# Performance work log

Hardware: AMD Instinct MI355X
Metric: run time of the kernel (lower is better)

Reference implementation:

```python
import jax, jax.numpy as jnp
import numpy as np

SEQ, B, V, E, H, L, S_SRC = 128, 32, 32000, 1024, 1024, 3, 64


def setup_inputs() -> dict:
    key = jax.random.key(0)
    ks = jax.random.split(key, 8)
    sc = 0.05
    return {
        "tokens": jax.random.randint(ks[0], (SEQ, B), 0, V),
        "emb_W": jax.random.normal(ks[1], (V, E), jnp.float32) * 0.1,
        "W_ih": jax.random.normal(ks[2], (L, 4 * H, E), jnp.float32) * sc,
        "W_hh": jax.random.normal(ks[3], (L, 4 * H, H), jnp.float32) * sc,
        "b_ih": jnp.zeros((L, 4 * H), jnp.float32),
        "b_hh": jnp.zeros((L, 4 * H), jnp.float32),
        "attn_Win": jax.random.normal(ks[4], (E, E), jnp.float32) * sc,
        "attn_Wout": jax.random.normal(ks[5], (E, 2 * E), jnp.float32) * sc,
        "final_b": jnp.zeros((V,), jnp.float32),
        "encoder_outs": jax.random.normal(ks[6], (S_SRC, B, E), jnp.float32),
        "h0": jnp.zeros((L, B, H), jnp.float32),
        "c0": jnp.zeros((L, B, H), jnp.float32),
    }


def reference(tokens, emb_W, W_ih, W_hh, b_ih, b_hh, attn_Win, attn_Wout,
              final_b, encoder_outs, h0, c0):
    # Eval mode: all dropouts (dropoute/i/h/out) are identity.
    emb = emb_W[tokens]                                  # [SEQ, B, E]
    ctx = jnp.transpose(encoder_outs, (1, 0, 2))         # [B, S_src, E]

    def lstm_cell(x, h, c, l):
        gates = x @ W_ih[l].T + b_ih[l] + h @ W_hh[l].T + b_hh[l]  # [B, 4H]
        i, f, g, o = jnp.split(gates, 4, axis=-1)        # torch order: i,f,g,o
        i, f, o = jax.nn.sigmoid(i), jax.nn.sigmoid(f), jax.nn.sigmoid(o)
        g = jnp.tanh(g)
        c_new = f * c + i * g
        return o * jnp.tanh(c_new), c_new

    def step(carry, x_t):
        h, c = carry                                     # each [L, B, H]
        hs, cs = [], []
        inp = x_t
        for l in range(L):
            h_new, c_new = lstm_cell(inp, h[l], c[l], l)
            hs.append(h_new)
            cs.append(c_new)
            inp = h_new                                  # dropouth is identity
        # SoftDotAttention on last layer hidden
        target = h_new @ attn_Win.T                      # [B, E]
        attn = jax.nn.softmax(jnp.einsum('bse,be->bs', ctx, target), axis=-1)
        wc = jnp.einsum('bs,bse->be', attn, ctx)         # weighted context
        h_tilde = jnp.tanh(jnp.concatenate([wc, h_new], axis=-1) @ attn_Wout.T)
        return (jnp.stack(hs), jnp.stack(cs)), h_tilde

    (_, _), outs = jax.lax.scan(step, (h0, c0), emb)     # outs: [SEQ, B, E]
    logits = outs @ emb_W.T + final_b                    # tied weights: [SEQ, B, V]
    return logits
```

## Files before the change

### kernel.cpp

```cpp
#include <hip/hip_runtime.h>
#include <cstdint>
#include <cstddef>

#define SEQ   128
#define BB    32
#define EE    1024
#define HH    1024
#define G4    4096
#define VV    32000
#define NROWS 4096

typedef _Float16 h16x8 __attribute__((ext_vector_type(8)));
typedef _Float16 h16x4 __attribute__((ext_vector_type(4)));
typedef float f32x4  __attribute__((ext_vector_type(4)));

#define AS_G(p) ((const __attribute__((address_space(1))) void*)(p))
#define AS_L(p) ((__attribute__((address_space(3))) void*)(p))

__device__ __forceinline__ float sigmf(float x) { return 1.0f / (1.0f + expf(-x)); }

#define OFF_SYNC    0ull
#define OFF_HFRAG   40960ull
#define OFF_EMB     434176ull
#define OFF_X0      8822784ull
#define OFF_WIH0    42377216ull
#define OFF_WP4     50765824ull
#define OFF_WP0     84320256ull
#define OFF_EMBW    92708864ull
#define OFF_WIN     158244864ull
#define OFF_WOUT    160342016ull
#define OFF_ENC     164536320ull
#define OFF_H2ALL   168730624ull
#define OFF_CONCAT  177119232ull
#define OFF_TARGET  193896448ull
#define OFF_HT      202285056ull
#define WS_NEEDED   210673664ull

__global__ __launch_bounds__(256) void k_conv(const float* __restrict__ s,
                                              _Float16* __restrict__ d, int n4) {
  int i = blockIdx.x * blockDim.x + threadIdx.x;
  int st = gridDim.x * blockDim.x;
  for (; i < n4; i += st) {
    float4 v = ((const float4*)s)[i];
    h16x4 o; o[0] = (_Float16)v.x; o[1] = (_Float16)v.y; o[2] = (_Float16)v.z; o[3] = (_Float16)v.w;
    ((h16x4*)d)[i] = o;
  }
}

__global__ __launch_bounds__(256) void k_gather(const int* __restrict__ tok,
                                                const float* __restrict__ embW,
                                                _Float16* __restrict__ emb) {
  int row = blockIdx.x;
  int t = tok[row];
  float4 v = ((const float4*)(embW + (size_t)t * EE))[threadIdx.x];
  h16x4 o; o[0] = (_Float16)v.x; o[1] = (_Float16)v.y; o[2] = (_Float16)v.z; o[3] = (_Float16)v.w;
  ((h16x4*)(emb + (size_t)row * EE))[threadIdx.x] = o;
}

__global__ __launch_bounds__(256) void k_packw4(const float* __restrict__ Wih,
                                                const float* __restrict__ Whh,
                                                _Float16* __restrict__ out) {
  int i = blockIdx.x * blockDim.x + threadIdx.x;
  int st = gridDim.x * blockDim.x;
  const int total = 256 * 65536;
  for (; i < total; i += st) {
    int w = i >> 16, rem = i & 65535;
    int mat = rem >> 14, jj = (rem >> 10) & 15, k = rem & 1023;
    int layer = 1 + (mat >> 1), isHH = mat & 1;
    int row = ((jj >> 2) << 10) + (w << 2) + (jj & 3);
    int ks = k ^ ((jj & 7) << 3);
    const float* src = (isHH ? Whh : Wih) + (size_t)layer * G4 * 1024 + (size_t)row * 1024 + ks;
    out[i] = (_Float16)(*src);
  }
}

__global__ __launch_bounds__(256) void k_packw0(const float* __restrict__ Whh,
                                                _Float16* __restrict__ out) {
  int i = blockIdx.x * blockDim.x + threadIdx.x;
  int st = gridDim.x * blockDim.x;
  const int total = 256 * 16384;
  for (; i < total; i += st) {
    int w = i >> 14, rem = i & 16383;
    int ks = rem >> 9, lane = (rem >> 3) & 63, e = rem & 7;
    int jj = lane & 15, q = lane >> 4;
    int row = ((jj >> 2) << 10) + (w << 2) + (jj & 3);
    int k = ks * 32 + q * 8 + e;
    out[i] = (_Float16)Whh[(size_t)row * 1024 + k];
  }
}

__global__ __launch_bounds__(256) void k_init(const float* __restrict__ h0,
                                              _Float16* __restrict__ hfrag,
                                              unsigned* __restrict__ sync) {
  int i = blockIdx.x * blockDim.x + threadIdx.x;
  if (i < 64 + 8192) sync[i] = 0u;
  if (i >= 3 * BB * HH) return;
  int l = i >> 15, rem = i & 32767;
  int b = rem >> 10, n = rem & 1023;
  int parI = (l == 1) ? 0 : 1;
  int tbb = b >> 4, ks = n >> 5, q = (n >> 3) & 3, e = n & 7;
  int lane2 = (b & 15) | (q << 4);
  hfrag[(size_t)(l * 2 + parI) * 32768 + ((size_t)(tbb * 32 + ks) * 64 + lane2) * 8 + e] =
      (_Float16)h0[i];
}

template <int EPI>
__global__ __launch_bounds__(256) void k_gemm(const _Float16* __restrict__ A,
                                              const _Float16* __restrict__ B,
                                              void* __restrict__ C, int M, int N, int K,
                                              const float* __restrict__ bias1,
                                              const float* __restrict__ bias2) {
  __shared__ _Float16 As[2][128 * 32];
  __shared__ _Float16 Bs[2][128 * 32];
  const int ntn = N / 128;
  const int nwg = gridDim.x;
  const int bid = (blockIdx.x & 7) * (nwg >> 3) + (blockIdx.x >> 3);
  const int tm = bid / ntn, tn = bid % ntn;
  const int tid = threadIdx.x, lane = tid & 63;
  const int wv = tid >> 6, wr = wv >> 1, wc = wv & 1;
  f32x4 acc[4][4] = {};

  auto stage = [&](int buf, int k0) {
#pragma unroll
    for (int i = 0; i < 2; ++i) {
      int eo = (i * 256 + tid) * 8;
      int r = eo >> 5, c = eo & 31;
      __builtin_amdgcn_global_load_lds(AS_G(A + (size_t)(tm * 128 + r) * K + k0 + c),
                                       AS_L(&As[buf][eo]), 16, 0, 0);
      __builtin_amdgcn_global_load_lds(AS_G(B + (size_t)(tn * 128 + r) * K + k0 + c),
                                       AS_L(&Bs[buf][eo]), 16, 0, 0);
    }
  };
  stage(0, 0);
  __syncthreads();
  const int nk = K / 32;
  for (int kt = 0; kt < nk; ++kt) {
    if (kt + 1 < nk) stage((kt + 1) & 1, (kt + 1) * 32);
    const int buf = kt & 1;
    h16x8 af[4], bfr[4];
#pragma unroll
    for (int mi = 0; mi < 4; ++mi)
      af[mi] = *(const h16x8*)&As[buf][(wr * 64 + mi * 16 + (lane & 15)) * 32 + (lane >> 4) * 8];
#pragma unroll
    for (int ni = 0; ni < 4; ++ni)
      bfr[ni] = *(const h16x8*)&Bs[buf][(wc * 64 + ni * 16 + (lane & 15)) * 32 + (lane >> 4) * 8];
#pragma unroll
    for (int mi = 0; mi < 4; ++mi)
#pragma unroll
      for (int ni = 0; ni < 4; ++ni)
        acc[mi][ni] = __builtin_amdgcn_mfma_f32_16x16x32_f16(af[mi], bfr[ni], acc[mi][ni], 0, 0, 0);
    __syncthreads();
  }
  const int rbase = tm * 128 + wr * 64;
  const int cbase = tn * 128 + wc * 64;
#pragma unroll
  for (int mi = 0; mi < 4; ++mi) {
#pragma unroll
    for (int ni = 0; ni < 4; ++ni) {
#pragma unroll
      for (int r = 0; r < 4; ++r) {
        int mm = rbase + mi * 16 + (lane >> 4) * 4 + r;
        int nn = cbase + ni * 16 + (lane & 15);
        float v = acc[mi][ni][r];
        if (EPI == 1) {
          ((_Float16*)C)[(size_t)mm * N + nn] = (_Float16)v;
        } else {
          ((_Float16*)C)[(size_t)mm * N + nn] = (_Float16)tanhf(v);
        }
      }
    }
  }
}

template <int EPI>
__global__ __launch_bounds__(512, 2) void k_gemm256(const _Float16* __restrict__ A,
                                                    const _Float16* __restrict__ B,
                                                    void* __restrict__ C, int M, int N, int K,
                                                    const float* __restrict__ bias1,
                                                    const float* __restrict__ bias2) {
  extern __shared__ char glds[];
  _Float16* Asl = (_Float16*)glds;
  _Float16* Bsl = (_Float16*)(glds + 3 * 8192 * 2);
  const int ntn = N / 256;
  const int nwg = gridDim.x;
  const int bid = (blockIdx.x & 7) * (nwg >> 3) + (blockIdx.x >> 3);
  const int tm = bid / ntn, tn = bid % ntn;
  const int tid = threadIdx.x, lane = tid & 63;
  const int wid = tid >> 6, wm = wid >> 2, wn = wid & 3;
  const int fr = lane & 15, fc = lane >> 4;
  const int srow0 = tid >> 2, sg = tid & 3;

  f32x4 acc[8][4] = {};
  const int nt = K / 32;

  auto stage = [&](int t) {
    const int slot = t % 3;
    const size_t kof = (size_t)t * 32 + sg * 8;
#pragma unroll
    for (int r = 0; r < 2; ++r) {
      int row = r * 128 + srow0;
      __builtin_amdgcn_global_load_lds(AS_G(A + (size_t)(tm * 256 + row) * K + kof),
                                       AS_L(&Asl[slot * 8192 + row * 32 + sg * 8]), 16, 0, 0);
    }
#pragma unroll
    for (int r = 0; r < 2; ++r) {
      int row = r * 128 + srow0;
      __builtin_amdgcn_global_load_lds(AS_G(B + (size_t)(tn * 256 + row) * K + kof),
                                       AS_L(&Bsl[slot * 8192 + row * 32 + sg * 8]), 16, 0, 0);
    }
  };

  stage(0);
  stage(1);
  asm volatile("s_waitcnt vmcnt(4)" ::: "memory");
  asm volatile("s_barrier" ::: "memory");

  for (int t = 0; t < nt; ++t) {
    if (t + 2 < nt) {
      stage(t + 2);
      asm volatile("s_waitcnt vmcnt(4)" ::: "memory");
    } else {
      asm volatile("s_waitcnt vmcnt(0)" ::: "memory");
    }
    asm volatile("s_barrier" ::: "memory");
    const int slot = t % 3;
    const _Float16* as = &Asl[slot * 8192];
    const _Float16* bs = &Bsl[slot * 8192];
    h16x8 af[8], bf[4];
#pragma unroll
    for (int mi = 0; mi < 8; ++mi)
      af[mi] = *(const h16x8*)&as[(wm * 128 + mi * 16 + fr) * 32 + fc * 8];
#pragma unroll
    for (int ni = 0; ni < 4; ++ni)
      bf[ni] = *(const h16x8*)&bs[(wn * 64 + ni * 16 + fr) * 32 + fc * 8];
    __builtin_amdgcn_s_setprio(1);
#pragma unroll
    for (int mi = 0; mi < 8; ++mi)
#pragma unroll
      for (int ni = 0; ni < 4; ++ni)
        acc[mi][ni] = __builtin_amdgcn_mfma_f32_16x16x32_f16(af[mi], bf[ni], acc[mi][ni], 0, 0, 0);
    __builtin_amdgcn_s_setprio(0);
    asm volatile("s_barrier" ::: "memory");
  }

  const int rbase = tm * 256 + wm * 128;
  const int cbase = tn * 256 + wn * 64;
#pragma unroll
  for (int mi = 0; mi < 8; ++mi) {
#pragma unroll
    for (int ni = 0; ni < 4; ++ni) {
#pragma unroll
      for (int r = 0; r < 4; ++r) {
        int mm = rbase + mi * 16 + fc * 4 + r;
        int nn = cbase + ni * 16 + fr;
        float v = acc[mi][ni][r];
        if (EPI == 0) {
          ((float*)C)[(size_t)mm * N + nn] = v + bias1[nn];
        } else {
          ((_Float16*)C)[(size_t)mm * N + nn] = (_Float16)(v + bias1[nn] + bias2[nn]);
        }
      }
    }
  }
}

__global__ __launch_bounds__(512) void k_recur(const _Float16* __restrict__ Wp4,
                                               const _Float16* __restrict__ Wp0,
                                               const _Float16* __restrict__ X0bf,
                                               _Float16* __restrict__ hfrag,
                                               _Float16* __restrict__ h2all,
                                               _Float16* __restrict__ concat,
                                               const float* __restrict__ bih,
                                               const float* __restrict__ bhh,
                                               const float* __restrict__ c0p,
                                               unsigned* __restrict__ sync) {
  extern __shared__ char lds[];
  _Float16* ldsW = (_Float16*)lds;
  float* redbuf = (float*)(lds + 131072);
  _Float16* hstage = (_Float16*)(lds + 131072);
  float* gbuf = (float*)(lds + 149504);
  unsigned* arrive = sync + 64;

  const int w = blockIdx.x;
  const int tid = threadIdx.x, lane = tid & 63, wv = tid >> 6;
  const int tb = wv & 1, kq = wv >> 1;
  const int row = (lane >> 4) * 4, col = lane & 15;

  for (int i = 0; i < 16; ++i) {
    int eo = (i * 512 + tid) * 8;
    *(h16x8*)&ldsW[eo] = *(const h16x8*)(Wp4 + (size_t)w * 65536 + eo);
  }
  h16x8 w0reg[8];
#pragma unroll
  for (int i = 0; i < 8; ++i)
    w0reg[i] = *(const h16x8*)(Wp0 + (size_t)w * 16384 + ((size_t)(kq * 8 + i) * 64 + lane) * 8);

  const int eb = tid >> 2, eni = tid & 3, en = w * 4 + eni;
  float c0r = 0.f, c1r = 0.f, c2r = 0.f;
  float b1r[4] = {0, 0, 0, 0}, b2r[4] = {0, 0, 0, 0};
  if (tid < 128) {
    c0r = c0p[0 * BB * HH + eb * HH + en];
    c1r = c0p[1 * BB * HH + eb * HH + en];
    c2r = c0p[2 * BB * HH + eb * HH + en];
#pragma unroll
    for (int g = 0; g < 4; ++g) {
      b1r[g] = bih[1 * G4 + g * 1024 + en] + bhh[1 * G4 + g * 1024 + en];
      b2r[g] = bih[2 * G4 + g * 1024 + en] + bhh[2 * G4 + g * 1024 + en];
    }
  }
  const int pk_l = tid >> 5, pk_r = tid & 31;
  const size_t pk_idx = ((size_t)(((pk_r >> 4) * 32 + (w >> 3)) * 64 + (pk_r & 15) +
                                  (((w >> 1) & 3) << 4))) * 8 + 4 * (w & 1);
  __syncthreads();

  for (int tau = 0; tau < 130; ++tau) {
    const int p = tau & 1;
    const _Float16* h0r = hfrag + (size_t)(0 + (1 - p)) * 32768;
    const _Float16* h1r = hfrag + (size_t)(2 + (1 - p)) * 32768;
    const _Float16* h2r = hfrag + (size_t)(4 + (1 - p)) * 32768;

    h16x8 a0[8], a1[8], a2[8];
#pragma unroll
    for (int i = 0; i < 8; ++i) {
      int ks = kq * 8 + i;
      size_t off = ((size_t)(tb * 32 + ks) * 64 + lane) * 8;
      a0[i] = *(const h16x8*)(h0r + off);
      a1[i] = *(const h16x8*)(h1r + off);
      a2[i] = *(const h16x8*)(h2r + off);
    }
    float xg0 = 0.f, xg1 = 0.f, xg2 = 0.f, xg3 = 0.f;
    if (tid < 128 && tau < 128) {
      size_t xb = ((size_t)(tau * BB + eb)) * G4 + en;
      xg0 = (float)X0bf[xb];        xg1 = (float)X0bf[xb + 1024];
      xg2 = (float)X0bf[xb + 2048]; xg3 = (float)X0bf[xb + 3072];
    }
    f32x4 acc0 = {}, acc1 = {}, acc2 = {};
#pragma unroll
    for (int i = 0; i < 8; ++i) {
      int ks = kq * 8 + i;
      int jj = lane & 15, q = lane >> 4;
      int kk = (ks * 32 + q * 8) ^ ((jj & 7) << 3);
      const h16x8 bw1i = *(const h16x8*)&ldsW[0 * 16384 + jj * 1024 + kk];
      const h16x8 bw1h = *(const h16x8*)&ldsW[1 * 16384 + jj * 1024 + kk];
      const h16x8 bw2i = *(const h16x8*)&ldsW[2 * 16384 + jj * 1024 + kk];
      const h16x8 bw2h = *(const h16x8*)&ldsW[3 * 16384 + jj * 1024 + kk];
      acc0 = __builtin_amdgcn_mfma_f32_16x16x32_f16(a0[i], w0reg[i], acc0, 0, 0, 0);
      acc1 = __builtin_amdgcn_mfma_f32_16x16x32_f16(a0[i], bw1i, acc1, 0, 0, 0);
      acc1 = __builtin_amdgcn_mfma_f32_16x16x32_f16(a1[i], bw1h, acc1, 0, 0, 0);
      acc2 = __builtin_amdgcn_mfma_f32_16x16x32_f16(a1[i], bw2i, acc2, 0, 0, 0);
      acc2 = __builtin_amdgcn_mfma_f32_16x16x32_f16(a2[i], bw2h, acc2, 0, 0, 0);
    }
    if (kq >= 1) {
      int s = kq - 1;
#pragma unroll
      for (int r = 0; r < 4; ++r) {
        redbuf[((0 * 3 + s) * 2 + tb) * 256 + (row + r) * 16 + col] = acc0[r];
        redbuf[((1 * 3 + s) * 2 + tb) * 256 + (row + r) * 16 + col] = acc1[r];
        redbuf[((2 * 3 + s) * 2 + tb) * 256 + (row + r) * 16 + col] = acc2[r];
      }
    }
    __syncthreads();
    if (kq == 0) {
#pragma unroll
      for (int r = 0; r < 4; ++r) {
        float v0 = acc0[r], v1 = acc1[r], v2 = acc2[r];
#pragma unroll
        for (int s = 0; s < 3; ++s) {
          v0 += redbuf[((0 * 3 + s) * 2 + tb) * 256 + (row + r) * 16 + col];
          v1 += redbuf[((1 * 3 + s) * 2 + tb) * 256 + (row + r) * 16 + col];
          v2 += redbuf[((2 * 3 + s) * 2 + tb) * 256 + (row + r) * 16 + col];
        }
        gbuf[(0 * 32 + tb * 16 + row + r) * 16 + col] = v0;
        gbuf[(1 * 32 + tb * 16 + row + r) * 16 + col] = v1;
        gbuf[(2 * 32 + tb * 16 + row + r) * 16 + col] = v2;
      }
    }
    __syncthreads();
    if (tid < 128) {
      if (tau < 128) {
        float gi = gbuf[(0 * 32 + eb) * 16 + eni] + xg0;
        float gf = gbuf[(0 * 32 + eb) * 16 + 4 + eni] + xg1;
        float gg = gbuf[(0 * 32 + eb) * 16 + 8 + eni] + xg2;
        float go = gbuf[(0 * 32 + eb) * 16 + 12 + eni] + xg3;
        c0r = sigmf(gf) * c0r + sigmf(gi) * tanhf(gg);
        hstage[0 * 128 + tid] = (_Float16)(sigmf(go) * tanhf(c0r));
      }
      if (tau >= 1 && tau < 129) {
        float gi = gbuf[(1 * 32 + eb) * 16 + eni] + b1r[0];
        float gf = gbuf[(1 * 32 + eb) * 16 + 4 + eni] + b1r[1];
        float gg = gbuf[(1 * 32 + eb) * 16 + 8 + eni] + b1r[2];
        float go = gbuf[(1 * 32 + eb) * 16 + 12 + eni] + b1r[3];
        c1r = sigmf(gf) * c1r + sigmf(gi) * tanhf(gg);
        hstage[1 * 128 + tid] = (_Float16)(sigmf(go) * tanhf(c1r));
      }
      if (tau >= 2) {
        float gi = gbuf[(2 * 32 + eb) * 16 + eni] + b2r[0];
        float gf = gbuf[(2 * 32 + eb) * 16 + 4 + eni] + b2r[1];
        float gg = gbuf[(2 * 32 + eb) * 16 + 8 + eni] + b2r[2];
        float go = gbuf[(2 * 32 + eb) * 16 + 12 + eni] + b2r[3];
        c2r = sigmf(gf) * c2r + sigmf(gi) * tanhf(gg);
        float h = sigmf(go) * tanhf(c2r);
        _Float16 hb = (_Float16)h;
        hstage[2 * 128 + tid] = hb;
        int t2 = tau - 2;
        h2all[(size_t)(t2 * BB + eb) * HH + en] = hb;
        concat[(size_t)(t2 * BB + eb) * 2048 + 1024 + en] = hb;
      }
    }
    __syncthreads();
    {
      bool act = (tid < 96) &&
                 ((pk_l == 0) ? (tau < 128)
                  : (pk_l == 1) ? (tau >= 1 && tau < 129) : (tau >= 2));
      if (act) {
        unsigned long long v = *(const unsigned long long*)&hstage[pk_l * 128 + pk_r * 4];
        __hip_atomic_store(
            (unsigned long long*)(hfrag + (size_t)(pk_l * 2 + p) * 32768 + pk_idx), v,
            __ATOMIC_RELAXED, __HIP_MEMORY_SCOPE_AGENT);
      }
      asm volatile("s_waitcnt vmcnt(0)" ::: "memory");
    }
    __syncthreads();
    if (tid == 0)
      __hip_atomic_store(&arrive[w * 32], (unsigned)(tau + 1), __ATOMIC_RELAXED,
                         __HIP_MEMORY_SCOPE_AGENT);
    if (tau < 129) {
      if (tid < 64) {
        for (;;) {
          bool ok = true;
#pragma unroll
          for (int j = 0; j < 4; ++j) {
            unsigned v = __hip_atomic_load(&arrive[(tid * 4 + j) * 32], __ATOMIC_RELAXED,
                                           __HIP_MEMORY_SCOPE_AGENT);
            ok &= (v >= (unsigned)(tau + 1));
          }
          if (__all(ok)) break;
          __builtin_amdgcn_s_sleep(1);
        }
        __builtin_amdgcn_fence(__ATOMIC_ACQUIRE, "agent");
      }
      __syncthreads();
    }
  }
}

__global__ __launch_bounds__(256) void k_attn(const _Float16* __restrict__ target,
                                              const _Float16* __restrict__ encb,
                                              _Float16* __restrict__ concat) {
  __shared__ float sc[64];
  __shared__ float att[64];
  int m = blockIdx.x, b = m & 31;
  int tid = threadIdx.x, lane = tid & 63, wv = tid >> 6;
  const h16x8* tp = (const h16x8*)(target + (size_t)m * EE + lane * 16);
  h16x8 tg0 = tp[0], tg1 = tp[1];
  for (int si = 0; si < 16; ++si) {
    int s = wv * 16 + si;
    const h16x8* ep = (const h16x8*)(encb + ((size_t)s * BB + b) * EE + lane * 16);
    h16x8 e0 = ep[0], e1 = ep[1];
    float a = 0.f;
#pragma unroll
    for (int j = 0; j < 8; ++j) a += (float)e0[j] * (float)tg0[j];
#pragma unroll
    for (int j = 0; j < 8; ++j) a += (float)e1[j] * (float)tg1[j];
#pragma unroll
    for (int off = 32; off >= 1; off >>= 1) a += __shfl_xor(a, off);
    if (lane == 0) sc[s] = a;
  }
  __syncthreads();
  if (wv == 0) {
    float v = sc[lane], mx = v;
#pragma unroll
    for (int off = 32; off >= 1; off >>= 1) mx = fmaxf(mx, __shfl_xor(mx, off));
    float e = expf(v - mx), sm = e;
#pragma unroll
    for (int off = 32; off >= 1; off >>= 1) sm += __shfl_xor(sm, off);
    att[lane] = e / sm;
  }
  __syncthreads();
  int e4 = tid * 4;
  float a0 = 0, a1 = 0, a2 = 0, a3 = 0;
  for (int s = 0; s < 64; ++s) {
    float wgt = att[s];
    h16x4 ev = *(const h16x4*)(encb + ((size_t)s * BB + b) * EE + e4);
    a0 += wgt * (float)ev[0]; a1 += wgt * (float)ev[1];
    a2 += wgt * (float)ev[2]; a3 += wgt * (float)ev[3];
  }
  h16x4 o; o[0] = (_Float16)a0; o[1] = (_Float16)a1; o[2] = (_Float16)a2; o[3] = (_Float16)a3;
  *(h16x4*)(concat + (size_t)m * 2048 + e4) = o;
}

extern "C" void kernel_launch(void* const* d_in, const int* in_sizes, int n_in,
                              void* d_out, int out_size, void* d_ws, size_t ws_size,
                              hipStream_t stream) {
  const int* tokens = (const int*)d_in[0];
  const float* embW = (const float*)d_in[1];
  const float* Wih = (const float*)d_in[2];
  const float* Whh = (const float*)d_in[3];
  const float* bih = (const float*)d_in[4];
  const float* bhh = (const float*)d_in[5];
  const float* Win = (const float*)d_in[6];
  const float* Wout = (const float*)d_in[7];
  const float* finalb = (const float*)d_in[8];
  const float* enc = (const float*)d_in[9];
  const float* h0 = (const float*)d_in[10];
  const float* c0 = (const float*)d_in[11];
  (void)in_sizes; (void)n_in; (void)out_size;
  if (ws_size < WS_NEEDED) return;

  char* ws = (char*)d_ws;
  unsigned* sync = (unsigned*)(ws + OFF_SYNC);
  _Float16* hfrag = (_Float16*)(ws + OFF_HFRAG);
  _Float16* emb = (_Float16*)(ws + OFF_EMB);
  _Float16* X0bf = (_Float16*)(ws + OFF_X0);
  _Float16* Wih0b = (_Float16*)(ws + OFF_WIH0);
  _Float16* Wp4 = (_Float16*)(ws + OFF_WP4);
  _Float16* Wp0 = (_Float16*)(ws + OFF_WP0);
  _Float16* embWb = (_Float16*)(ws + OFF_EMBW);
  _Float16* Winb = (_Float16*)(ws + OFF_WIN);
  _Float16* Woutb = (_Float16*)(ws + OFF_WOUT);
  _Float16* encb = (_Float16*)(ws + OFF_ENC);
  _Float16* h2all = (_Float16*)(ws + OFF_H2ALL);
  _Float16* concat = (_Float16*)(ws + OFF_CONCAT);
  _Float16* target = (_Float16*)(ws + OFF_TARGET);
  _Float16* ht = (_Float16*)(ws + OFF_HT);

  const unsigned LDSB = 155648;
  const unsigned LDSG = 98304;
  static int lds_set = 0;
  if (!lds_set) {
    hipFuncSetAttribute((const void*)k_recur, hipFuncAttributeMaxDynamicSharedMemorySize,
                        (int)LDSB);
    hipFuncSetAttribute((const void*)k_gemm256<0>, hipFuncAttributeMaxDynamicSharedMemorySize,
                        (int)LDSG);
    hipFuncSetAttribute((const void*)k_gemm256<1>, hipFuncAttributeMaxDynamicSharedMemorySize,
                        (int)LDSG);
    lds_set = 1;
  }

  k_conv<<<4096, 256, 0, stream>>>(embW, embWb, VV * EE / 4);
  k_conv<<<1024, 256, 0, stream>>>(Wih, Wih0b, G4 * EE / 4);
  k_conv<<<512, 256, 0, stream>>>(Win, Winb, EE * EE / 4);
  k_conv<<<512, 256, 0, stream>>>(Wout, Woutb, EE * 2048 / 4);
  k_conv<<<512, 256, 0, stream>>>(enc, encb, 64 * BB * EE / 4);
  k_gather<<<NROWS, 256, 0, stream>>>(tokens, embW, emb);
  k_packw4<<<8192, 256, 0, stream>>>(Wih, Whh, Wp4);
  k_packw0<<<4096, 256, 0, stream>>>(Whh, Wp0);
  k_init<<<384, 256, 0, stream>>>(h0, hfrag, sync);

  k_gemm256<1><<<16 * 16, 512, LDSG, stream>>>(emb, Wih0b, X0bf, NROWS, G4, EE, bih, bhh);

  k_recur<<<256, 512, LDSB, stream>>>(Wp4, Wp0, X0bf, hfrag, h2all, concat,
                                      bih, bhh, c0, sync);

  k_gemm<1><<<32 * 8, 256, 0, stream>>>(h2all, Winb, target, NROWS, EE, EE, nullptr, nullptr);
  k_attn<<<NROWS, 256, 0, stream>>>(target, encb, concat);
  k_gemm<2><<<32 * 8, 256, 0, stream>>>(concat, Woutb, ht, NROWS, EE, 2048, nullptr, nullptr);

  k_gemm256<0><<<16 * 125, 512, LDSG, stream>>>(ht, embWb, d_out, NROWS, VV, EE, finalb, nullptr);
}
```

Before: 1.637 ms.

## Use per-timestep hidden-state buffers to drop acquire fence; XCD-aware column mapping

The ping-pong hidden-state exchange buffer in the persistent recurrent kernel becomes a separate write-once buffer per timestep, placed in workspace regions that are dead during the recurrence. Because each buffer is never read before it is written, the kernel replaces the agent-scope acquire fence after the grid barrier with a compiler-only barrier. This is meant to avoid the cache invalidation cost on every one of the 130 steps. Block-to-hidden-column assignment is also permuted so that blocks likely resident on the same XCD own contiguous columns, and the weight packing kernels are updated to match. The change relies on no stale cache lines existing for fresh addresses. That is a subtle memory-model assumption that could break correctness.

Result: faster. 1.425 ms (-13.0%).

```diff
diff --git a/kernel.cpp b/kernel.cpp
--- a/kernel.cpp
+++ b/kernel.cpp
@@ -20,21 +20,22 @@
 __device__ __forceinline__ float sigmf(float x) { return 1.0f / (1.0f + expf(-x)); }
 
 #define OFF_SYNC    0ull
-#define OFF_HFRAG   40960ull
-#define OFF_EMB     434176ull
-#define OFF_X0      8822784ull
-#define OFF_WIH0    42377216ull
-#define OFF_WP4     50765824ull
-#define OFF_WP0     84320256ull
-#define OFF_EMBW    92708864ull
-#define OFF_WIN     158244864ull
-#define OFF_WOUT    160342016ull
-#define OFF_ENC     164536320ull
-#define OFF_H2ALL   168730624ull
-#define OFF_CONCAT  177119232ull
-#define OFF_TARGET  193896448ull
-#define OFF_HT      202285056ull
-#define WS_NEEDED   210673664ull
+#define OFF_HFRAG0  40960ull
+#define OFF_EMB     630784ull
+#define OFF_WIH0    9019392ull
+#define OFF_TARGET  17408000ull
+#define OFF_HT      25796608ull
+#define OFF_HFRAGH  630784ull
+#define OFF_X0      34185216ull
+#define OFF_WP4     67739648ull
+#define OFF_WP0     101294080ull
+#define OFF_EMBW    109682688ull
+#define OFF_WIN     175218688ull
+#define OFF_WOUT    177315840ull
+#define OFF_ENC     181510144ull
+#define OFF_H2ALL   185704448ull
+#define OFF_CONCAT  194093056ull
+#define WS_NEEDED   210870272ull
 
 __global__ __launch_bounds__(256) void k_conv(const float* __restrict__ s,
                                               _Float16* __restrict__ d, int n4) {
@@ -65,9 +66,10 @@
   const int total = 256 * 65536;
   for (; i < total; i += st) {
     int w = i >> 16, rem = i & 65535;
+    int wp = (w & 7) * 32 + (w >> 3);
     int mat = rem >> 14, jj = (rem >> 10) & 15, k = rem & 1023;
     int layer = 1 + (mat >> 1), isHH = mat & 1;
-    int row = ((jj >> 2) << 10) + (w << 2) + (jj & 3);
+    int row = ((jj >> 2) << 10) + (wp << 2) + (jj & 3);
     int ks = k ^ ((jj & 7) << 3);
     const float* src = (isHH ? Whh : Wih) + (size_t)layer * G4 * 1024 + (size_t)row * 1024 + ks;
     out[i] = (_Float16)(*src);
@@ -81,26 +83,26 @@
   const int total = 256 * 16384;
   for (; i < total; i += st) {
     int w = i >> 14, rem = i & 16383;
+    int wp = (w & 7) * 32 + (w >> 3);
     int ks = rem >> 9, lane = (rem >> 3) & 63, e = rem & 7;
     int jj = lane & 15, q = lane >> 4;
-    int row = ((jj >> 2) << 10) + (w << 2) + (jj & 3);
+    int row = ((jj >> 2) << 10) + (wp << 2) + (jj & 3);
     int k = ks * 32 + q * 8 + e;
     out[i] = (_Float16)Whh[(size_t)row * 1024 + k];
   }
 }
 
 __global__ __launch_bounds__(256) void k_init(const float* __restrict__ h0,
-                                              _Float16* __restrict__ hfrag,
+                                              _Float16* __restrict__ hfrag0,
                                               unsigned* __restrict__ sync) {
   int i = blockIdx.x * blockDim.x + threadIdx.x;
   if (i < 64 + 8192) sync[i] = 0u;
   if (i >= 3 * BB * HH) return;
   int l = i >> 15, rem = i & 32767;
   int b = rem >> 10, n = rem & 1023;
-  int parI = (l == 1) ? 0 : 1;
   int tbb = b >> 4, ks = n >> 5, q = (n >> 3) & 3, e = n & 7;
   int lane2 = (b & 15) | (q << 4);
-  hfrag[(size_t)(l * 2 + parI) * 32768 + ((size_t)(tbb * 32 + ks) * 64 + lane2) * 8 + e] =
+  hfrag0[(size_t)l * 131072 + ((size_t)(tbb * 32 + ks) * 64 + lane2) * 8 + e] =
       (_Float16)h0[i];
 }
 
@@ -267,7 +269,8 @@
 __global__ __launch_bounds__(512) void k_recur(const _Float16* __restrict__ Wp4,
                                                const _Float16* __restrict__ Wp0,
                                                const _Float16* __restrict__ X0bf,
-                                               _Float16* __restrict__ hfrag,
+                                               _Float16* __restrict__ hfrag0,
+                                               _Float16* __restrict__ hfragH,
                                                _Float16* __restrict__ h2all,
                                                _Float16* __restrict__ concat,
                                                const float* __restrict__ bih,
@@ -282,6 +285,7 @@
   unsigned* arrive = sync + 64;
 
   const int w = blockIdx.x;
+  const int wp = (w & 7) * 32 + (w >> 3);
   const int tid = threadIdx.x, lane = tid & 63, wv = tid >> 6;
   const int tb = wv & 1, kq = wv >> 1;
   const int row = (lane >> 4) * 4, col = lane & 15;
@@ -295,7 +299,7 @@
   for (int i = 0; i < 8; ++i)
     w0reg[i] = *(const h16x8*)(Wp0 + (size_t)w * 16384 + ((size_t)(kq * 8 + i) * 64 + lane) * 8);
 
-  const int eb = tid >> 2, eni = tid & 3, en = w * 4 + eni;
+  const int eb = tid >> 2, eni = tid & 3, en = wp * 4 + eni;
   float c0r = 0.f, c1r = 0.f, c2r = 0.f;
   float b1r[4] = {0, 0, 0, 0}, b2r[4] = {0, 0, 0, 0};
   if (tid < 128) {
@@ -309,15 +313,18 @@
     }
   }
   const int pk_l = tid >> 5, pk_r = tid & 31;
-  const size_t pk_idx = ((size_t)(((pk_r >> 4) * 32 + (w >> 3)) * 64 + (pk_r & 15) +
-                                  (((w >> 1) & 3) << 4))) * 8 + 4 * (w & 1);
+  const size_t pk_idx = ((size_t)(((pk_r >> 4) * 32 + (wp >> 3)) * 64 + (pk_r & 15) +
+                                  (((wp >> 1) & 3) << 4))) * 8 + 4 * (wp & 1);
   __syncthreads();
 
   for (int tau = 0; tau < 130; ++tau) {
-    const int p = tau & 1;
-    const _Float16* h0r = hfrag + (size_t)(0 + (1 - p)) * 32768;
-    const _Float16* h1r = hfrag + (size_t)(2 + (1 - p)) * 32768;
-    const _Float16* h2r = hfrag + (size_t)(4 + (1 - p)) * 32768;
+    const _Float16* rb = (tau < 3) ? (hfrag0 + (size_t)tau * 98304)
+                                   : (hfragH + (size_t)(tau - 3) * 98304);
+    _Float16* wb = (tau + 1 < 3) ? (hfrag0 + (size_t)(tau + 1) * 98304)
+                                 : (hfragH + (size_t)(tau - 2) * 98304);
+    const _Float16* h0r = rb;
+    const _Float16* h1r = rb + 32768;
+    const _Float16* h2r = rb + 65536;
 
     h16x8 a0[8], a1[8], a2[8];
 #pragma unroll
@@ -411,11 +418,12 @@
     {
       bool act = (tid < 96) &&
                  ((pk_l == 0) ? (tau < 128)
-                  : (pk_l == 1) ? (tau >= 1 && tau < 129) : (tau >= 2));
+                  : (pk_l == 1) ? (tau >= 1 && tau < 129)
+                                : (tau >= 2 && tau < 129));
       if (act) {
         unsigned long long v = *(const unsigned long long*)&hstage[pk_l * 128 + pk_r * 4];
         __hip_atomic_store(
-            (unsigned long long*)(hfrag + (size_t)(pk_l * 2 + p) * 32768 + pk_idx), v,
+            (unsigned long long*)(wb + (size_t)pk_l * 32768 + pk_idx), v,
             __ATOMIC_RELAXED, __HIP_MEMORY_SCOPE_AGENT);
       }
       asm volatile("s_waitcnt vmcnt(0)" ::: "memory");
@@ -437,7 +445,7 @@
           if (__all(ok)) break;
           __builtin_amdgcn_s_sleep(1);
         }
-        __builtin_amdgcn_fence(__ATOMIC_ACQUIRE, "agent");
+        asm volatile("" ::: "memory");
       }
       __syncthreads();
     }
@@ -509,7 +517,8 @@
 
   char* ws = (char*)d_ws;
   unsigned* sync = (unsigned*)(ws + OFF_SYNC);
-  _Float16* hfrag = (_Float16*)(ws + OFF_HFRAG);
+  _Float16* hfrag0 = (_Float16*)(ws + OFF_HFRAG0);
+  _Float16* hfragH = (_Float16*)(ws + OFF_HFRAGH);
   _Float16* emb = (_Float16*)(ws + OFF_EMB);
   _Float16* X0bf = (_Float16*)(ws + OFF_X0);
   _Float16* Wih0b = (_Float16*)(ws + OFF_WIH0);
@@ -545,11 +554,11 @@
   k_gather<<<NROWS, 256, 0, stream>>>(tokens, embW, emb);
   k_packw4<<<8192, 256, 0, stream>>>(Wih, Whh, Wp4);
   k_packw0<<<4096, 256, 0, stream>>>(Whh, Wp0);
-  k_init<<<384, 256, 0, stream>>>(h0, hfrag, sync);
+  k_init<<<384, 256, 0, stream>>>(h0, hfrag0, sync);
 
   k_gemm256<1><<<16 * 16, 512, LDSG, stream>>>(emb, Wih0b, X0bf, NROWS, G4, EE, bih, bhh);
 
-  k_recur<<<256, 512, LDSB, stream>>>(Wp4, Wp0, X0bf, hfrag, h2all, concat,
+  k_recur<<<256, 512, LDSB, stream>>>(Wp4, Wp0, X0bf, hfrag0, hfragH, h2all, concat,
                                       bih, bhh, c0, sync);
 
   k_gemm<1><<<32 * 8, 256, 0, stream>>>(h2all, Winb, target, NROWS, EE, EE, nullptr, nullptr);
```
